# Optimization experiments

Hardware: AMD Instinct MI355X
Metric: run time of the kernel (lower is better)

Reference implementation:

```python
import jax, jax.numpy as jnp
import numpy as np
from functools import reduce

# 2x2 beamsplitter gate (1/sqrt(2)) * [[1, i], [i, 1]]
BS_2x2 = (1.0 / np.sqrt(2.0)) * np.array([[1 + 0j, 0 + 1j], [0 + 1j, 1 + 0j]], dtype=np.complex64)


def _kron_phase_diag(a, b):
    """Diagonal vector of kron_i diag([e^{i a_i}, e^{i b_i}]) -> shape (2^n,) complex64.

    Mathematically identical to building the dense Kronecker diagonal matrix
    (as the original tf.linalg.LinearOperatorKronecker(...).to_dense()) and
    right-multiplying by it, since M @ diag(d) == M * d.
    """
    pairs = jnp.stack([jnp.exp(1j * a), jnp.exp(1j * b)], axis=1)  # (n, 2)
    n = pairs.shape[0]
    vec = pairs[0]
    for i in range(1, n):  # static small loop over qubits
        vec = jnp.kron(vec, pairs[i])
    return vec


def _bs_full(n):
    # Dense n-fold Kronecker product of the 2x2 beamsplitter, (2^n, 2^n) complex64
    return reduce(jnp.kron, [jnp.asarray(BS_2x2)] * n)


def setup_inputs() -> dict:
    key = jax.random.key(0)
    kx, ka, kb, kt, kp = jax.random.split(key, 5)
    n = 12
    N = 2 ** n
    batch = 64
    two_pi = 2.0 * np.pi
    return {
        "x": jax.random.normal(kx, (batch, 2, N), dtype=jnp.float32),
        "alphas": jax.random.uniform(ka, (n,), dtype=jnp.float32) * two_pi,
        "betas": jax.random.uniform(kb, (n,), dtype=jnp.float32) * two_pi,
        "thetas": jax.random.uniform(kt, (n,), dtype=jnp.float32) * two_pi,
        "phis": jax.random.uniform(kp, (n,), dtype=jnp.float32) * two_pi,
    }


def reference(x, alphas, betas, thetas, phis):
    n = alphas.shape[0]
    bs = _bs_full(n)                                   # (N, N) complex64
    d_in = _kron_phase_diag(alphas, betas)             # (N,)
    d_theta = _kron_phase_diag(thetas, jnp.zeros_like(thetas))
    d_phi = _kron_phase_diag(phis, jnp.zeros_like(phis))

    out = jax.lax.complex(x[:, 0, :], x[:, 1, :])      # (B, N) complex64
    out = (out * d_in) @ bs                            # input phase shifts + beamsplitter
    out = (out * d_theta) @ bs                         # theta shifts + beamsplitter
    out = out * d_phi                                  # final phi shifts
    return jnp.stack([out.real, out.imag], axis=1)     # (B, 2, N) float32
```

## Files before the change

kernel.cpp:

```cpp
#include <hip/hip_runtime.h>
#include <math.h>

#define NN 4096
#define BLK 512
#define EPT 8
#define PADSZ (NN + (NN >> 3))

__device__ __forceinline__ void cmul(float& ar, float& ai, float br, float bi) {
    float nr = ar * br - ai * bi;
    float ni = ar * bi + ai * br;
    ar = nr; ai = ni;
}

__device__ __forceinline__ void bfly_pair(float* vr, float* vi, int a, int b) {
    float ur = vr[a], ui = vi[a], wr = vr[b], wi = vi[b];
    vr[a] = ur - wi; vi[a] = ui + wr;
    vr[b] = wr - ui; vi[b] = wi + ur;
}

__device__ __forceinline__ void bfly3(float* vr, float* vi) {
    bfly_pair(vr, vi, 0, 1); bfly_pair(vr, vi, 2, 3); bfly_pair(vr, vi, 4, 5); bfly_pair(vr, vi, 6, 7);
    bfly_pair(vr, vi, 0, 2); bfly_pair(vr, vi, 1, 3); bfly_pair(vr, vi, 4, 6); bfly_pair(vr, vi, 5, 7);
    bfly_pair(vr, vi, 0, 4); bfly_pair(vr, vi, 1, 5); bfly_pair(vr, vi, 2, 6); bfly_pair(vr, vi, 3, 7);
}

template<int P>
__device__ __forceinline__ int jidx(int t, int r) {
    return ((t >> P) << (P + 3)) | (r << P) | (t & ((1 << P) - 1));
}

template<int PC, int PN, bool CROSS>
__device__ __forceinline__ void exchange(float2* buf, float* vr, float* vi, int t) {
    #pragma unroll
    for (int r = 0; r < EPT; ++r) {
        int j = jidx<PC>(t, r);
        buf[j + (j >> 3)] = make_float2(vr[r], vi[r]);
    }
    if (CROSS) { __syncthreads(); }
    else       { asm volatile("" ::: "memory"); }
    #pragma unroll
    for (int r = 0; r < EPT; ++r) {
        int j = jidx<PN>(t, r);
        float2 v = buf[j + (j >> 3)];
        vr[r] = v.x; vi[r] = v.y;
    }
}

__global__ __launch_bounds__(BLK) void qubit_layer_kernel(
    const float* __restrict__ x,
    const float* __restrict__ alphas, const float* __restrict__ betas,
    const float* __restrict__ thetas, const float* __restrict__ phis,
    float* __restrict__ out)
{
    __shared__ float2 B1[PADSZ];
    __shared__ float2 B2[PADSZ];
    __shared__ float2 tbl[6][64];

    const int t = threadIdx.x;
    const int b = blockIdx.x;

    if (t < 384) {
        int part = t >> 6, idx = t & 63, set = part >> 1, half = part & 1;
        float a = 0.f;
        #pragma unroll
        for (int m = 0; m < 6; ++m) {
            int q = half ? m : (6 + m);
            int bit = (idx >> (5 - m)) & 1;
            float av, bv;
            if (set == 0)      { av = alphas[q]; bv = betas[q]; }
            else if (set == 1) { av = thetas[q]; bv = 0.f; }
            else               { av = phis[q];   bv = 0.f; }
            a += bit ? bv : av;
        }
        float s, c;
        __sincosf(a, &s, &c);
        float sc = (set >= 1 && half == 0) ? (1.0f / 64.0f) : 1.0f;
        tbl[part][idx] = make_float2(c * sc, s * sc);
    }

    const float* xr = x + (size_t)b * 2 * NN;
    const float* xi = xr + NN;
    float vr[EPT], vi[EPT];
    {
        float4 a0 = ((const float4*)(xr + t * EPT))[0];
        float4 a1 = ((const float4*)(xr + t * EPT))[1];
        float4 c0 = ((const float4*)(xi + t * EPT))[0];
        float4 c1 = ((const float4*)(xi + t * EPT))[1];
        vr[0]=a0.x; vr[1]=a0.y; vr[2]=a0.z; vr[3]=a0.w; vr[4]=a1.x; vr[5]=a1.y; vr[6]=a1.z; vr[7]=a1.w;
        vi[0]=c0.x; vi[1]=c0.y; vi[2]=c0.z; vi[3]=c0.w; vi[4]=c1.x; vi[5]=c1.y; vi[6]=c1.z; vi[7]=c1.w;
    }
    __syncthreads();

    {
        float2 eh = tbl[1][t >> 3];
        const float4* elv = (const float4*)&tbl[0][(t & 7) << 3];
        #pragma unroll
        for (int k = 0; k < 4; ++k) {
            float4 e2 = elv[k];
            float er0 = e2.x, ei0 = e2.y, er1 = e2.z, ei1 = e2.w;
            cmul(er0, ei0, eh.x, eh.y);
            cmul(er1, ei1, eh.x, eh.y);
            cmul(vr[2*k],   vi[2*k],   er0, ei0);
            cmul(vr[2*k+1], vi[2*k+1], er1, ei1);
        }
    }

    bfly3(vr, vi);
    exchange<0, 3, false>(B1, vr, vi, t); bfly3(vr, vi);
    exchange<3, 6, false>(B1, vr, vi, t); bfly3(vr, vi);
    exchange<6, 9, true >(B1, vr, vi, t); bfly3(vr, vi);

    {
        float2 el = tbl[2][t & 63];
        #pragma unroll
        for (int r = 0; r < EPT; ++r) {
            float2 eh = tbl[3][(t >> 6) + (r << 3)];
            float er = el.x, ei = el.y;
            cmul(er, ei, eh.x, eh.y);
            cmul(vr[r], vi[r], er, ei);
        }
    }

    bfly3(vr, vi);
    exchange<9, 6, true >(B2, vr, vi, t); bfly3(vr, vi);
    exchange<6, 3, false>(B1, vr, vi, t); bfly3(vr, vi);
    exchange<3, 0, false>(B1, vr, vi, t); bfly3(vr, vi);

    {
        float2 eh = tbl[5][t >> 3];
        const float4* elv = (const float4*)&tbl[4][(t & 7) << 3];
        #pragma unroll
        for (int k = 0; k < 4; ++k) {
            float4 e2 = elv[k];
            float er0 = e2.x, ei0 = e2.y, er1 = e2.z, ei1 = e2.w;
            cmul(er0, ei0, eh.x, eh.y);
            cmul(er1, ei1, eh.x, eh.y);
            cmul(vr[2*k],   vi[2*k],   er0, ei0);
            cmul(vr[2*k+1], vi[2*k+1], er1, ei1);
        }
    }
    float* outr = out + (size_t)b * 2 * NN;
    float* outi = outr + NN;
    {
        ((float4*)(outr + t * EPT))[0] = make_float4(vr[0], vr[1], vr[2], vr[3]);
        ((float4*)(outr + t * EPT))[1] = make_float4(vr[4], vr[5], vr[6], vr[7]);
        ((float4*)(outi + t * EPT))[0] = make_float4(vi[0], vi[1], vi[2], vi[3]);
        ((float4*)(outi + t * EPT))[1] = make_float4(vi[4], vi[5], vi[6], vi[7]);
    }
}

extern "C" void kernel_launch(void* const* d_in, const int* in_sizes, int n_in,
                              void* d_out, int out_size, void* d_ws, size_t ws_size,
                              hipStream_t stream) {
    const float* x      = (const float*)d_in[0];
    const float* alphas = (const float*)d_in[1];
    const float* betas  = (const float*)d_in[2];
    const float* thetas = (const float*)d_in[3];
    const float* phis   = (const float*)d_in[4];
    float* out = (float*)d_out;

    const int batch = in_sizes[0] / (2 * NN);
    qubit_layer_kernel<<<batch, BLK, 0, stream>>>(x, alphas, betas, thetas, phis, out);
}
```

Baseline: 10.26 us.

## Switch to radix-16 butterflies with 256 threads and swizzled single LDS buffer

Each thread now holds 16 elements and applies 4 qubit butterflies per register pass, so each 12-qubit transform takes 3 stages and 2 LDS exchanges instead of 4 stages and 3. The padded double buffer is replaced by one XOR-swizzled buffer, and the global loads are issued before the phase-table setup so they overlap it. The cost is higher register pressure and half as many threads per block, which may reduce occupancy and latency hiding with only 64 blocks launched.

Result: slower. 11.63 us (+13.4%).

```diff
diff --git a/kernel.cpp b/kernel.cpp
--- a/kernel.cpp
+++ b/kernel.cpp
@@ -2,9 +2,8 @@
 #include <math.h>
 
 #define NN 4096
-#define BLK 512
-#define EPT 8
-#define PADSZ (NN + (NN >> 3))
+#define BLK 256
+#define EPT 16
 
 __device__ __forceinline__ void cmul(float& ar, float& ai, float br, float bi) {
     float nr = ar * br - ai * bi;
@@ -18,30 +17,38 @@
     vr[b] = wr - ui; vi[b] = wi + ur;
 }
 
-__device__ __forceinline__ void bfly3(float* vr, float* vi) {
-    bfly_pair(vr, vi, 0, 1); bfly_pair(vr, vi, 2, 3); bfly_pair(vr, vi, 4, 5); bfly_pair(vr, vi, 6, 7);
-    bfly_pair(vr, vi, 0, 2); bfly_pair(vr, vi, 1, 3); bfly_pair(vr, vi, 4, 6); bfly_pair(vr, vi, 5, 7);
-    bfly_pair(vr, vi, 0, 4); bfly_pair(vr, vi, 1, 5); bfly_pair(vr, vi, 2, 6); bfly_pair(vr, vi, 3, 7);
+__device__ __forceinline__ void bfly4(float* vr, float* vi) {
+    #pragma unroll
+    for (int m = 0; m < 4; ++m) {
+        #pragma unroll
+        for (int a = 0; a < 16; ++a) {
+            if (!(a & (1 << m))) bfly_pair(vr, vi, a, a | (1 << m));
+        }
+    }
 }
 
 template<int P>
 __device__ __forceinline__ int jidx(int t, int r) {
-    return ((t >> P) << (P + 3)) | (r << P) | (t & ((1 << P) - 1));
+    return ((t >> P) << (P + 4)) | (r << P) | (t & ((1 << P) - 1));
 }
 
-template<int PC, int PN, bool CROSS>
-__device__ __forceinline__ void exchange(float2* buf, float* vr, float* vi, int t) {
+__device__ __forceinline__ int swz(int j) { return j ^ ((j >> 4) & 15); }
+
+template<int P>
+__device__ __forceinline__ void wrt(float2* buf, const float* vr, const float* vi, int t) {
     #pragma unroll
     for (int r = 0; r < EPT; ++r) {
-        int j = jidx<PC>(t, r);
-        buf[j + (j >> 3)] = make_float2(vr[r], vi[r]);
+        int j = jidx<P>(t, r);
+        buf[swz(j)] = make_float2(vr[r], vi[r]);
     }
-    if (CROSS) { __syncthreads(); }
-    else       { asm volatile("" ::: "memory"); }
+}
+
+template<int P>
+__device__ __forceinline__ void rd(const float2* buf, float* vr, float* vi, int t) {
     #pragma unroll
     for (int r = 0; r < EPT; ++r) {
-        int j = jidx<PN>(t, r);
-        float2 v = buf[j + (j >> 3)];
+        int j = jidx<P>(t, r);
+        float2 v = buf[swz(j)];
         vr[r] = v.x; vi[r] = v.y;
     }
 }
@@ -52,15 +59,26 @@
     const float* __restrict__ thetas, const float* __restrict__ phis,
     float* __restrict__ out)
 {
-    __shared__ float2 B1[PADSZ];
-    __shared__ float2 B2[PADSZ];
+    __shared__ float2 S[NN];
     __shared__ float2 tbl[6][64];
 
     const int t = threadIdx.x;
     const int b = blockIdx.x;
 
-    if (t < 384) {
-        int part = t >> 6, idx = t & 63, set = part >> 1, half = part & 1;
+    const float* xr = x + (size_t)b * 2 * NN;
+    const float* xi = xr + NN;
+    float4 La0 = ((const float4*)(xr + t * EPT))[0];
+    float4 La1 = ((const float4*)(xr + t * EPT))[1];
+    float4 La2 = ((const float4*)(xr + t * EPT))[2];
+    float4 La3 = ((const float4*)(xr + t * EPT))[3];
+    float4 Lb0 = ((const float4*)(xi + t * EPT))[0];
+    float4 Lb1 = ((const float4*)(xi + t * EPT))[1];
+    float4 Lb2 = ((const float4*)(xi + t * EPT))[2];
+    float4 Lb3 = ((const float4*)(xi + t * EPT))[3];
+
+    #pragma unroll
+    for (int e = t; e < 384; e += BLK) {
+        int part = e >> 6, idx = e & 63, set = part >> 1, half = part & 1;
         float a = 0.f;
         #pragma unroll
         for (int m = 0; m < 6; ++m) {
@@ -77,25 +95,23 @@
         float sc = (set >= 1 && half == 0) ? (1.0f / 64.0f) : 1.0f;
         tbl[part][idx] = make_float2(c * sc, s * sc);
     }
-
-    const float* xr = x + (size_t)b * 2 * NN;
-    const float* xi = xr + NN;
-    float vr[EPT], vi[EPT];
-    {
-        float4 a0 = ((const float4*)(xr + t * EPT))[0];
-        float4 a1 = ((const float4*)(xr + t * EPT))[1];
-        float4 c0 = ((const float4*)(xi + t * EPT))[0];
-        float4 c1 = ((const float4*)(xi + t * EPT))[1];
-        vr[0]=a0.x; vr[1]=a0.y; vr[2]=a0.z; vr[3]=a0.w; vr[4]=a1.x; vr[5]=a1.y; vr[6]=a1.z; vr[7]=a1.w;
-        vi[0]=c0.x; vi[1]=c0.y; vi[2]=c0.z; vi[3]=c0.w; vi[4]=c1.x; vi[5]=c1.y; vi[6]=c1.z; vi[7]=c1.w;
-    }
     __syncthreads();
 
+    float vr[EPT], vi[EPT];
+    vr[0]=La0.x; vr[1]=La0.y; vr[2]=La0.z; vr[3]=La0.w;
+    vr[4]=La1.x; vr[5]=La1.y; vr[6]=La1.z; vr[7]=La1.w;
+    vr[8]=La2.x; vr[9]=La2.y; vr[10]=La2.z; vr[11]=La2.w;
+    vr[12]=La3.x; vr[13]=La3.y; vr[14]=La3.z; vr[15]=La3.w;
+    vi[0]=Lb0.x; vi[1]=Lb0.y; vi[2]=Lb0.z; vi[3]=Lb0.w;
+    vi[4]=Lb1.x; vi[5]=Lb1.y; vi[6]=Lb1.z; vi[7]=Lb1.w;
+    vi[8]=Lb2.x; vi[9]=Lb2.y; vi[10]=Lb2.z; vi[11]=Lb2.w;
+    vi[12]=Lb3.x; vi[13]=Lb3.y; vi[14]=Lb3.z; vi[15]=Lb3.w;
+
     {
-        float2 eh = tbl[1][t >> 3];
-        const float4* elv = (const float4*)&tbl[0][(t & 7) << 3];
+        float2 eh = tbl[1][t >> 2];
+        const float4* elv = (const float4*)&tbl[0][(t & 3) << 4];
         #pragma unroll
-        for (int k = 0; k < 4; ++k) {
+        for (int k = 0; k < 8; ++k) {
             float4 e2 = elv[k];
             float er0 = e2.x, ei0 = e2.y, er1 = e2.z, ei1 = e2.w;
             cmul(er0, ei0, eh.x, eh.y);
@@ -105,32 +121,43 @@
         }
     }
 
-    bfly3(vr, vi);
-    exchange<0, 3, false>(B1, vr, vi, t); bfly3(vr, vi);
-    exchange<3, 6, false>(B1, vr, vi, t); bfly3(vr, vi);
-    exchange<6, 9, true >(B1, vr, vi, t); bfly3(vr, vi);
+    bfly4(vr, vi);
+    wrt<0>(S, vr, vi, t);
+    asm volatile("" ::: "memory");
+    rd<4>(S, vr, vi, t);
+    bfly4(vr, vi);
+    wrt<4>(S, vr, vi, t);
+    __syncthreads();
+    rd<8>(S, vr, vi, t);
+    bfly4(vr, vi);
 
     {
         float2 el = tbl[2][t & 63];
         #pragma unroll
         for (int r = 0; r < EPT; ++r) {
-            float2 eh = tbl[3][(t >> 6) + (r << 3)];
+            float2 eh = tbl[3][(r << 2) | (t >> 6)];
             float er = el.x, ei = el.y;
             cmul(er, ei, eh.x, eh.y);
             cmul(vr[r], vi[r], er, ei);
         }
     }
 
-    bfly3(vr, vi);
-    exchange<9, 6, true >(B2, vr, vi, t); bfly3(vr, vi);
-    exchange<6, 3, false>(B1, vr, vi, t); bfly3(vr, vi);
-    exchange<3, 0, false>(B1, vr, vi, t); bfly3(vr, vi);
+    bfly4(vr, vi);
+    __syncthreads();
+    wrt<8>(S, vr, vi, t);
+    __syncthreads();
+    rd<4>(S, vr, vi, t);
+    bfly4(vr, vi);
+    wrt<4>(S, vr, vi, t);
+    asm volatile("" ::: "memory");
+    rd<0>(S, vr, vi, t);
+    bfly4(vr, vi);
 
     {
-        float2 eh = tbl[5][t >> 3];
-        const float4* elv = (const float4*)&tbl[4][(t & 7) << 3];
+        float2 eh = tbl[5][t >> 2];
+        const float4* elv = (const float4*)&tbl[4][(t & 3) << 4];
         #pragma unroll
-        for (int k = 0; k < 4; ++k) {
+        for (int k = 0; k < 8; ++k) {
             float4 e2 = elv[k];
             float er0 = e2.x, ei0 = e2.y, er1 = e2.z, ei1 = e2.w;
             cmul(er0, ei0, eh.x, eh.y);
@@ -141,12 +168,14 @@
     }
     float* outr = out + (size_t)b * 2 * NN;
     float* outi = outr + NN;
-    {
-        ((float4*)(outr + t * EPT))[0] = make_float4(vr[0], vr[1], vr[2], vr[3]);
-        ((float4*)(outr + t * EPT))[1] = make_float4(vr[4], vr[5], vr[6], vr[7]);
-        ((float4*)(outi + t * EPT))[0] = make_float4(vi[0], vi[1], vi[2], vi[3]);
-        ((float4*)(outi + t * EPT))[1] = make_float4(vi[4], vi[5], vi[6], vi[7]);
-    }
+    ((float4*)(outr + t * EPT))[0] = make_float4(vr[0], vr[1], vr[2], vr[3]);
+    ((float4*)(outr + t * EPT))[1] = make_float4(vr[4], vr[5], vr[6], vr[7]);
+    ((float4*)(outr + t * EPT))[2] = make_float4(vr[8], vr[9], vr[10], vr[11]);
+    ((float4*)(outr + t * EPT))[3] = make_float4(vr[12], vr[13], vr[14], vr[15]);
+    ((float4*)(outi + t * EPT))[0] = make_float4(vi[0], vi[1], vi[2], vi[3]);
+    ((float4*)(outi + t * EPT))[1] = make_float4(vi[4], vi[5], vi[6], vi[7]);
+    ((float4*)(outi + t * EPT))[2] = make_float4(vi[8], vi[9], vi[10], vi[11]);
+    ((float4*)(outi + t * EPT))[3] = make_float4(vi[12], vi[13], vi[14], vi[15]);
 }
 
 extern "C" void kernel_launch(void* const* d_in, const int* in_sizes, int n_in,
```

## Switch to radix-4 butterflies with 1024 threads and a single swizzled LDS buffer

Applied to the files above, without the earlier changes.

The Kronecker-beamsplitter transform now runs with 1024 threads per block, each holding 4 complex elements and applying radix-4 butterfly stages, instead of 512 threads with 8 elements and radix-8 stages. The two padded shared-memory buffers are replaced by one XOR-swizzled buffer, and the global input loads are issued before the phase-table computation to overlap their latency. This is meant to put more waves on each CU and lower per-thread register use. The cost is more exchange rounds through LDS and more block-wide barriers per sample.

Result: slower. 16.63 us (+62.1%).

```diff
diff --git a/kernel.cpp b/kernel.cpp
--- a/kernel.cpp
+++ b/kernel.cpp
@@ -2,9 +2,8 @@
 #include <math.h>
 
 #define NN 4096
-#define BLK 512
-#define EPT 8
-#define PADSZ (NN + (NN >> 3))
+#define BLK 1024
+#define EPT 4
 
 __device__ __forceinline__ void cmul(float& ar, float& ai, float br, float bi) {
     float nr = ar * br - ai * bi;
@@ -18,30 +17,33 @@
     vr[b] = wr - ui; vi[b] = wi + ur;
 }
 
-__device__ __forceinline__ void bfly3(float* vr, float* vi) {
-    bfly_pair(vr, vi, 0, 1); bfly_pair(vr, vi, 2, 3); bfly_pair(vr, vi, 4, 5); bfly_pair(vr, vi, 6, 7);
-    bfly_pair(vr, vi, 0, 2); bfly_pair(vr, vi, 1, 3); bfly_pair(vr, vi, 4, 6); bfly_pair(vr, vi, 5, 7);
-    bfly_pair(vr, vi, 0, 4); bfly_pair(vr, vi, 1, 5); bfly_pair(vr, vi, 2, 6); bfly_pair(vr, vi, 3, 7);
+__device__ __forceinline__ void bfly2(float* vr, float* vi) {
+    bfly_pair(vr, vi, 0, 1); bfly_pair(vr, vi, 2, 3);
+    bfly_pair(vr, vi, 0, 2); bfly_pair(vr, vi, 1, 3);
 }
 
 template<int P>
 __device__ __forceinline__ int jidx(int t, int r) {
-    return ((t >> P) << (P + 3)) | (r << P) | (t & ((1 << P) - 1));
+    return ((t >> P) << (P + 2)) | (r << P) | (t & ((1 << P) - 1));
 }
 
-template<int PC, int PN, bool CROSS>
-__device__ __forceinline__ void exchange(float2* buf, float* vr, float* vi, int t) {
+__device__ __forceinline__ int swz(int j) { return j ^ (((j >> 4) & 3) * 5); }
+
+template<int P>
+__device__ __forceinline__ void wrt(float2* buf, const float* vr, const float* vi, int t) {
     #pragma unroll
     for (int r = 0; r < EPT; ++r) {
-        int j = jidx<PC>(t, r);
-        buf[j + (j >> 3)] = make_float2(vr[r], vi[r]);
+        int j = jidx<P>(t, r);
+        buf[swz(j)] = make_float2(vr[r], vi[r]);
     }
-    if (CROSS) { __syncthreads(); }
-    else       { asm volatile("" ::: "memory"); }
+}
+
+template<int P>
+__device__ __forceinline__ void rd(const float2* buf, float* vr, float* vi, int t) {
     #pragma unroll
     for (int r = 0; r < EPT; ++r) {
-        int j = jidx<PN>(t, r);
-        float2 v = buf[j + (j >> 3)];
+        int j = jidx<P>(t, r);
+        float2 v = buf[swz(j)];
         vr[r] = v.x; vi[r] = v.y;
     }
 }
@@ -52,12 +54,16 @@
     const float* __restrict__ thetas, const float* __restrict__ phis,
     float* __restrict__ out)
 {
-    __shared__ float2 B1[PADSZ];
-    __shared__ float2 B2[PADSZ];
+    __shared__ float2 S[NN];
     __shared__ float2 tbl[6][64];
 
     const int t = threadIdx.x;
     const int b = blockIdx.x;
+
+    const float* xr = x + (size_t)b * 2 * NN;
+    const float* xi = xr + NN;
+    float4 La = *(const float4*)(xr + t * EPT);
+    float4 Lb = *(const float4*)(xi + t * EPT);
 
     if (t < 384) {
         int part = t >> 6, idx = t & 63, set = part >> 1, half = part & 1;
@@ -77,25 +83,17 @@
         float sc = (set >= 1 && half == 0) ? (1.0f / 64.0f) : 1.0f;
         tbl[part][idx] = make_float2(c * sc, s * sc);
     }
-
-    const float* xr = x + (size_t)b * 2 * NN;
-    const float* xi = xr + NN;
-    float vr[EPT], vi[EPT];
-    {
-        float4 a0 = ((const float4*)(xr + t * EPT))[0];
-        float4 a1 = ((const float4*)(xr + t * EPT))[1];
-        float4 c0 = ((const float4*)(xi + t * EPT))[0];
-        float4 c1 = ((const float4*)(xi + t * EPT))[1];
-        vr[0]=a0.x; vr[1]=a0.y; vr[2]=a0.z; vr[3]=a0.w; vr[4]=a1.x; vr[5]=a1.y; vr[6]=a1.z; vr[7]=a1.w;
-        vi[0]=c0.x; vi[1]=c0.y; vi[2]=c0.z; vi[3]=c0.w; vi[4]=c1.x; vi[5]=c1.y; vi[6]=c1.z; vi[7]=c1.w;
-    }
     __syncthreads();
 
+    float vr[EPT], vi[EPT];
+    vr[0]=La.x; vr[1]=La.y; vr[2]=La.z; vr[3]=La.w;
+    vi[0]=Lb.x; vi[1]=Lb.y; vi[2]=Lb.z; vi[3]=Lb.w;
+
     {
-        float2 eh = tbl[1][t >> 3];
-        const float4* elv = (const float4*)&tbl[0][(t & 7) << 3];
+        float2 eh = tbl[1][t >> 4];
+        const float4* elv = (const float4*)&tbl[0][(t & 15) << 2];
         #pragma unroll
-        for (int k = 0; k < 4; ++k) {
+        for (int k = 0; k < 2; ++k) {
             float4 e2 = elv[k];
             float er0 = e2.x, ei0 = e2.y, er1 = e2.z, ei1 = e2.w;
             cmul(er0, ei0, eh.x, eh.y);
@@ -105,32 +103,46 @@
         }
     }
 
-    bfly3(vr, vi);
-    exchange<0, 3, false>(B1, vr, vi, t); bfly3(vr, vi);
-    exchange<3, 6, false>(B1, vr, vi, t); bfly3(vr, vi);
-    exchange<6, 9, true >(B1, vr, vi, t); bfly3(vr, vi);
+    bfly2(vr, vi);
+    wrt<0>(S, vr, vi, t); asm volatile("" ::: "memory"); rd<2>(S, vr, vi, t);
+    bfly2(vr, vi);
+    wrt<2>(S, vr, vi, t); asm volatile("" ::: "memory"); rd<4>(S, vr, vi, t);
+    bfly2(vr, vi);
+    wrt<4>(S, vr, vi, t); asm volatile("" ::: "memory"); rd<6>(S, vr, vi, t);
+    bfly2(vr, vi);
+    wrt<6>(S, vr, vi, t); __syncthreads(); rd<8>(S, vr, vi, t);
+    bfly2(vr, vi);
+    wrt<8>(S, vr, vi, t); __syncthreads(); rd<10>(S, vr, vi, t);
+    bfly2(vr, vi);
 
     {
         float2 el = tbl[2][t & 63];
         #pragma unroll
         for (int r = 0; r < EPT; ++r) {
-            float2 eh = tbl[3][(t >> 6) + (r << 3)];
+            float2 eh = tbl[3][(r << 4) | (t >> 6)];
             float er = el.x, ei = el.y;
             cmul(er, ei, eh.x, eh.y);
             cmul(vr[r], vi[r], er, ei);
         }
     }
 
-    bfly3(vr, vi);
-    exchange<9, 6, true >(B2, vr, vi, t); bfly3(vr, vi);
-    exchange<6, 3, false>(B1, vr, vi, t); bfly3(vr, vi);
-    exchange<3, 0, false>(B1, vr, vi, t); bfly3(vr, vi);
+    bfly2(vr, vi);
+    wrt<10>(S, vr, vi, t); __syncthreads(); rd<8>(S, vr, vi, t);
+    bfly2(vr, vi);
+    wrt<8>(S, vr, vi, t); __syncthreads(); rd<6>(S, vr, vi, t);
+    bfly2(vr, vi);
+    wrt<6>(S, vr, vi, t); asm volatile("" ::: "memory"); rd<4>(S, vr, vi, t);
+    bfly2(vr, vi);
+    wrt<4>(S, vr, vi, t); asm volatile("" ::: "memory"); rd<2>(S, vr, vi, t);
+    bfly2(vr, vi);
+    wrt<2>(S, vr, vi, t); asm volatile("" ::: "memory"); rd<0>(S, vr, vi, t);
+    bfly2(vr, vi);
 
     {
-        float2 eh = tbl[5][t >> 3];
-        const float4* elv = (const float4*)&tbl[4][(t & 7) << 3];
+        float2 eh = tbl[5][t >> 4];
+        const float4* elv = (const float4*)&tbl[4][(t & 15) << 2];
         #pragma unroll
-        for (int k = 0; k < 4; ++k) {
+        for (int k = 0; k < 2; ++k) {
             float4 e2 = elv[k];
             float er0 = e2.x, ei0 = e2.y, er1 = e2.z, ei1 = e2.w;
             cmul(er0, ei0, eh.x, eh.y);
@@ -141,12 +153,8 @@
     }
     float* outr = out + (size_t)b * 2 * NN;
     float* outi = outr + NN;
-    {
-        ((float4*)(outr + t * EPT))[0] = make_float4(vr[0], vr[1], vr[2], vr[3]);
-        ((float4*)(outr + t * EPT))[1] = make_float4(vr[4], vr[5], vr[6], vr[7]);
-        ((float4*)(outi + t * EPT))[0] = make_float4(vi[0], vi[1], vi[2], vi[3]);
-        ((float4*)(outi + t * EPT))[1] = make_float4(vi[4], vi[5], vi[6], vi[7]);
-    }
+    *(float4*)(outr + t * EPT) = make_float4(vr[0], vr[1], vr[2], vr[3]);
+    *(float4*)(outi + t * EPT) = make_float4(vi[0], vi[1], vi[2], vi[3]);
 }
 
 extern "C" void kernel_launch(void* const* d_in, const int* in_sizes, int n_in,
```

## Pack shared-memory exchanges as bf16 complex with XOR swizzle and hoist global loads

Applied to the files above, without the earlier changes.

Intermediate values exchanged through LDS are now rounded to bf16 and packed as one 32-bit word per complex element instead of a float2. The padded layout is replaced by an XOR swizzle to avoid bank conflicts. The input loads are moved ahead of the phase-table computation so global latency overlaps the sincos work. This halves LDS traffic and footprint but adds precision loss at each of six exchanges, which may exceed tolerance.

New measurement: 10.75 us. 1.05x slower.

```diff
diff --git a/kernel.cpp b/kernel.cpp
--- a/kernel.cpp
+++ b/kernel.cpp
@@ -4,7 +4,6 @@
 #define NN 4096
 #define BLK 512
 #define EPT 8
-#define PADSZ (NN + (NN >> 3))
 
 __device__ __forceinline__ void cmul(float& ar, float& ai, float br, float bi) {
     float nr = ar * br - ai * bi;
@@ -29,20 +28,32 @@
     return ((t >> P) << (P + 3)) | (r << P) | (t & ((1 << P) - 1));
 }
 
+__device__ __forceinline__ int swz(int j) {
+    return j ^ ((j >> 5) & 31) ^ (((j >> 6) & 1) << 4);
+}
+
+__device__ __forceinline__ unsigned bfr(float f) {
+    unsigned u = __float_as_uint(f);
+    return (u + 0x7fffu + ((u >> 16) & 1u)) >> 16;
+}
+__device__ __forceinline__ unsigned packc(float re, float im) {
+    return bfr(re) | (bfr(im) << 16);
+}
+__device__ __forceinline__ float unlo(unsigned v) { return __uint_as_float(v << 16); }
+__device__ __forceinline__ float unhi(unsigned v) { return __uint_as_float(v & 0xffff0000u); }
+
 template<int PC, int PN, bool CROSS>
-__device__ __forceinline__ void exchange(float2* buf, float* vr, float* vi, int t) {
+__device__ __forceinline__ void exchange(unsigned* buf, float* vr, float* vi, int t) {
     #pragma unroll
     for (int r = 0; r < EPT; ++r) {
-        int j = jidx<PC>(t, r);
-        buf[j + (j >> 3)] = make_float2(vr[r], vi[r]);
+        buf[swz(jidx<PC>(t, r))] = packc(vr[r], vi[r]);
     }
     if (CROSS) { __syncthreads(); }
     else       { asm volatile("" ::: "memory"); }
     #pragma unroll
     for (int r = 0; r < EPT; ++r) {
-        int j = jidx<PN>(t, r);
-        float2 v = buf[j + (j >> 3)];
-        vr[r] = v.x; vi[r] = v.y;
+        unsigned v = buf[swz(jidx<PN>(t, r))];
+        vr[r] = unlo(v); vi[r] = unhi(v);
     }
 }
 
@@ -52,12 +63,19 @@
     const float* __restrict__ thetas, const float* __restrict__ phis,
     float* __restrict__ out)
 {
-    __shared__ float2 B1[PADSZ];
-    __shared__ float2 B2[PADSZ];
+    __shared__ unsigned S1[NN];
+    __shared__ unsigned S2[NN];
     __shared__ float2 tbl[6][64];
 
     const int t = threadIdx.x;
     const int b = blockIdx.x;
+
+    const float* xr = x + (size_t)b * 2 * NN;
+    const float* xi = xr + NN;
+    float4 a0 = ((const float4*)(xr + t * EPT))[0];
+    float4 a1 = ((const float4*)(xr + t * EPT))[1];
+    float4 c0 = ((const float4*)(xi + t * EPT))[0];
+    float4 c1 = ((const float4*)(xi + t * EPT))[1];
 
     if (t < 384) {
         int part = t >> 6, idx = t & 63, set = part >> 1, half = part & 1;
@@ -78,17 +96,10 @@
         tbl[part][idx] = make_float2(c * sc, s * sc);
     }
 
-    const float* xr = x + (size_t)b * 2 * NN;
-    const float* xi = xr + NN;
     float vr[EPT], vi[EPT];
-    {
-        float4 a0 = ((const float4*)(xr + t * EPT))[0];
-        float4 a1 = ((const float4*)(xr + t * EPT))[1];
-        float4 c0 = ((const float4*)(xi + t * EPT))[0];
-        float4 c1 = ((const float4*)(xi + t * EPT))[1];
-        vr[0]=a0.x; vr[1]=a0.y; vr[2]=a0.z; vr[3]=a0.w; vr[4]=a1.x; vr[5]=a1.y; vr[6]=a1.z; vr[7]=a1.w;
-        vi[0]=c0.x; vi[1]=c0.y; vi[2]=c0.z; vi[3]=c0.w; vi[4]=c1.x; vi[5]=c1.y; vi[6]=c1.z; vi[7]=c1.w;
-    }
+    vr[0]=a0.x; vr[1]=a0.y; vr[2]=a0.z; vr[3]=a0.w; vr[4]=a1.x; vr[5]=a1.y; vr[6]=a1.z; vr[7]=a1.w;
+    vi[0]=c0.x; vi[1]=c0.y; vi[2]=c0.z; vi[3]=c0.w; vi[4]=c1.x; vi[5]=c1.y; vi[6]=c1.z; vi[7]=c1.w;
+
     __syncthreads();
 
     {
@@ -106,9 +117,9 @@
     }
 
     bfly3(vr, vi);
-    exchange<0, 3, false>(B1, vr, vi, t); bfly3(vr, vi);
-    exchange<3, 6, false>(B1, vr, vi, t); bfly3(vr, vi);
-    exchange<6, 9, true >(B1, vr, vi, t); bfly3(vr, vi);
+    exchange<0, 3, false>(S1, vr, vi, t); bfly3(vr, vi);
+    exchange<3, 6, false>(S1, vr, vi, t); bfly3(vr, vi);
+    exchange<6, 9, true >(S1, vr, vi, t); bfly3(vr, vi);
 
     {
         float2 el = tbl[2][t & 63];
@@ -122,9 +133,9 @@
     }
 
     bfly3(vr, vi);
-    exchange<9, 6, true >(B2, vr, vi, t); bfly3(vr, vi);
-    exchange<6, 3, false>(B1, vr, vi, t); bfly3(vr, vi);
-    exchange<3, 0, false>(B1, vr, vi, t); bfly3(vr, vi);
+    exchange<9, 6, true >(S2, vr, vi, t); bfly3(vr, vi);
+    exchange<6, 3, false>(S1, vr, vi, t); bfly3(vr, vi);
+    exchange<3, 0, false>(S1, vr, vi, t); bfly3(vr, vi);
 
     {
         float2 eh = tbl[5][t >> 3];
@@ -141,12 +152,10 @@
     }
     float* outr = out + (size_t)b * 2 * NN;
     float* outi = outr + NN;
-    {
-        ((float4*)(outr + t * EPT))[0] = make_float4(vr[0], vr[1], vr[2], vr[3]);
-        ((float4*)(outr + t * EPT))[1] = make_float4(vr[4], vr[5], vr[6], vr[7]);
-        ((float4*)(outi + t * EPT))[0] = make_float4(vi[0], vi[1], vi[2], vi[3]);
-        ((float4*)(outi + t * EPT))[1] = make_float4(vi[4], vi[5], vi[6], vi[7]);
-    }
+    ((float4*)(outr + t * EPT))[0] = make_float4(vr[0], vr[1], vr[2], vr[3]);
+    ((float4*)(outr + t * EPT))[1] = make_float4(vr[4], vr[5], vr[6], vr[7]);
+    ((float4*)(outi + t * EPT))[0] = make_float4(vi[0], vi[1], vi[2], vi[3]);
+    ((float4*)(outi + t * EPT))[1] = make_float4(vi[4], vi[5], vi[6], vi[7]);
 }
 
 extern "C" void kernel_launch(void* const* d_in, const int* in_sizes, int n_in,
```
